# Kernel optimization log

Hardware: AMD Instinct MI355X
Metric: run time of the kernel (lower is better)

Reference implementation:

```python
import jax, jax.numpy as jnp
import numpy as np

B, S, H, IN, OUT, T = 1024, 256, 128, 2, 2, 512


def setup_inputs() -> dict:
    key = jax.random.key(0)
    ks = jax.random.split(key, 7)
    scale = 1.0 / np.sqrt(H)  # PyTorch LSTM init range ~ U(-1/sqrt(H), 1/sqrt(H))
    return {
        "x": jax.random.normal(ks[0], (B, S, IN), jnp.float32),
        "w_ih": jax.random.normal(ks[1], (4 * H, IN), jnp.float32) * scale,
        "w_hh": jax.random.normal(ks[2], (4 * H, H), jnp.float32) * scale,
        "b_ih": jax.random.normal(ks[3], (4 * H,), jnp.float32) * scale,
        "b_hh": jax.random.normal(ks[4], (4 * H,), jnp.float32) * scale,
        "w_fc": jax.random.normal(ks[5], (OUT, H), jnp.float32) * scale,
        "b_fc": jax.random.normal(ks[6], (OUT,), jnp.float32) * scale,
        "target_length": T,
    }


def reference(x, w_ih, w_hh, b_ih, b_hh, w_fc, b_fc, target_length):
    # PyTorch nn.LSTM cell, gate order (i, f, g, o). Dropout is identity (eval mode).
    bias = b_ih + b_hh
    hdim = w_hh.shape[1]

    def cell(h, c, x_t):
        gates = x_t @ w_ih.T + h @ w_hh.T + bias  # [B, 4H]
        i, f, g, o = jnp.split(gates, 4, axis=-1)
        c_new = jax.nn.sigmoid(f) * c + jax.nn.sigmoid(i) * jnp.tanh(g)
        h_new = jax.nn.sigmoid(o) * jnp.tanh(c_new)
        return h_new, c_new

    bsz = x.shape[0]
    h0 = jnp.zeros((bsz, hdim), x.dtype)
    c0 = jnp.zeros((bsz, hdim), x.dtype)

    # Encode input sequence
    def enc_step(carry, x_t):
        h, c = carry
        h, c = cell(h, c, x_t)
        return (h, c), None

    (h, c), _ = jax.lax.scan(enc_step, (h0, c0), jnp.swapaxes(x, 0, 1))

    inp0 = x[:, -1, :]  # [B, 2]

    def dec_step(carry, _):
        h, c, inp = carry
        h, c = cell(h, c, inp)
        pred = h @ w_fc.T + b_fc  # [B, 2]
        return (h, c, pred), pred

    _, preds = jax.lax.scan(dec_step, (h, c, inp0), None, length=target_length)
    return jnp.swapaxes(preds, 0, 1)  # [B, target_length, 2]
```

## Files before the change

kernel.cpp:

```cpp
#include <hip/hip_runtime.h>

typedef unsigned short ush;
typedef unsigned int uint32;
typedef __attribute__((ext_vector_type(8))) __bf16 bf16x8;
typedef __attribute__((ext_vector_type(4))) float f32x4;

#define NBLK 256
#define RB   4
#define NTHR 512
#define SENC 256
#define TDEC 512
#define HDIM 128
#define HSTR 144
#define XSTR 520
#define PSTR 1024

#define LOG2E  1.4426950408889634f
#define LOG2E2 2.8853900817779268f

__device__ __forceinline__ float bf2f(ush u){
  uint32 v = ((uint32)u) << 16;
  return __builtin_bit_cast(float, v);
}
__device__ __forceinline__ ush f2bf(float f){
  uint32 u = __builtin_bit_cast(uint32, f);
  u = (u + 0x7FFFu + ((u >> 16) & 1u)) >> 16;
  return (ush)u;
}
__device__ __forceinline__ float lo16f(uint32 w){ return __builtin_bit_cast(float, w << 16); }
__device__ __forceinline__ float hi16f(uint32 w){ return __builtin_bit_cast(float, w & 0xFFFF0000u); }

__device__ __forceinline__ float loadf(const void* p, int i, bool f32){
  return f32 ? ((const float*)p)[i] : bf2f(((const ush*)p)[i]);
}
__device__ __forceinline__ bf16x8 load8bf(const void* p, int i, bool f32){
  bf16x8 r;
  if (!f32){
    uint4 u = *reinterpret_cast<const uint4*>((const ush*)p + i);
    r = __builtin_bit_cast(bf16x8, u);
  } else {
    const float* fp = (const float*)p + i;
    #pragma unroll
    for (int j = 0; j < 8; ++j) r[j] = (__bf16)fp[j];
  }
  return r;
}
__device__ __forceinline__ float sigm(float x){
  return __builtin_amdgcn_rcpf(1.0f + __builtin_amdgcn_exp2f(-x * LOG2E));
}
__device__ __forceinline__ float tnh(float x){
  return 1.0f - 2.0f * __builtin_amdgcn_rcpf(__builtin_amdgcn_exp2f(x * LOG2E2) + 1.0f);
}
__device__ __forceinline__ f32x4 mfma4(const bf16x8* af, const bf16x8* b, f32x4 c){
  f32x4 r = __builtin_amdgcn_mfma_f32_16x16x32_bf16(af[0], b[0], c, 0, 0, 0);
  r = __builtin_amdgcn_mfma_f32_16x16x32_bf16(af[1], b[1], r, 0, 0, 0);
  r = __builtin_amdgcn_mfma_f32_16x16x32_bf16(af[2], b[2], r, 0, 0, 0);
  r = __builtin_amdgcn_mfma_f32_16x16x32_bf16(af[3], b[3], r, 0, 0, 0);
  return r;
}

__global__ void __launch_bounds__(NTHR, 2)
lstm_kernel(const void* __restrict__ xg,  const void* __restrict__ wih,
            const void* __restrict__ whh, const void* __restrict__ bih,
            const void* __restrict__ bhh, const void* __restrict__ wfc,
            const void* __restrict__ bfc, void* __restrict__ outg)
{
  __shared__ __attribute__((aligned(16))) ush x_lds[RB * XSTR];
  __shared__ __attribute__((aligned(16))) ush h_lds[2][RB * HSTR];
  __shared__ __attribute__((aligned(16))) ush pred_lds[RB][PSTR];

  const int tid   = threadIdx.x;
  const int lane  = tid & 63;
  const int wv    = tid >> 6;
  const int n     = lane & 15;
  const int q     = lane >> 4;
  const int gbase = wv << 4;
  const int blk   = blockIdx.x;

  const uint32* wp = (const uint32*)whh;
  int cnt = 0;
  #pragma unroll
  for (int i = 0; i < 64; ++i){
    uint32 e = (wp[i] >> 7) & 0xFFu;
    cnt += (e >= 90u && e <= 140u) ? 1 : 0;
  }
  const bool isf32 = (cnt < 40);

  for (int i = tid; i < 2 * RB * HSTR; i += NTHR) h_lds[0][i] = 0;

  if (!isf32){
    if (tid < 256){
      int row = tid >> 6, c = (tid & 63) * 8;
      uint4 v = *reinterpret_cast<const uint4*>((const ush*)xg + (blk * RB + row) * (SENC * 2) + c);
      *reinterpret_cast<uint4*>(&x_lds[row * XSTR + c]) = v;
    }
  } else {
    for (int i = tid; i < RB * SENC * 2; i += NTHR){
      int row = i >> 9, c = i & 511;
      x_lds[row * XSTR + c] = f2bf(((const float*)xg)[(blk * RB + row) * (SENC * 2) + c]);
    }
  }

  float wih0v[4], wih1v[4];
  f32x4 biasC[4];
  bf16x8 bfr[4][4];
  #pragma unroll
  for (int p = 0; p < 4; ++p){
    int g = p * 128 + gbase + n;
    float b = loadf(bih, g, isf32) + loadf(bhh, g, isf32);
    biasC[p][0] = b; biasC[p][1] = b; biasC[p][2] = b; biasC[p][3] = b;
    wih0v[p] = loadf(wih, g * 2 + 0, isf32);
    wih1v[p] = loadf(wih, g * 2 + 1, isf32);
    #pragma unroll
    for (int kk = 0; kk < 4; ++kk)
      bfr[p][kk] = load8bf(whh, g * HDIM + kk * 32 + q * 8, isf32);
  }
  bf16x8 wfcfr[4];
  #pragma unroll
  for (int kk = 0; kk < 4; ++kk){
    #pragma unroll
    for (int j = 0; j < 8; ++j){
      int k = kk * 32 + q * 8 + j;
      wfcfr[kk][j] = __builtin_bit_cast(__bf16, f2bf(loadf(wfc, (n & 1) * HDIM + k, isf32)));
    }
  }
  f32x4 pbfcC;
  {
    float pb = loadf(bfc, n & 1, isf32);
    pbfcC[0] = pb; pbfcC[1] = pb; pbfcC[2] = pb; pbfcC[3] = pb;
  }
  float wav[4], wbv[4];
  #pragma unroll
  for (int p = 0; p < 4; ++p){
    wav[p] = (n & 1) ? wih1v[p] : wih0v[p];
    wbv[p] = (n & 1) ? wih0v[p] : wih1v[p];
  }

  float cc = 0.0f;
  const int arow  = (n >> 2) * HSTR;
  const int hwofs = q * HSTR + gbase + n;
  int cur = 0;

  __syncthreads();

  #pragma unroll 1
  for (int s = 0; s <= SENC; ++s){
    int t = (s < SENC) ? s : SENC - 1;
    uint32 xw = *reinterpret_cast<const uint32*>(&x_lds[q * XSTR + t * 2]);
    float xa = lo16f(xw), xb = hi16f(xw);

    const ush* hb = &h_lds[cur][arow];
    bf16x8 af[4];
    #pragma unroll
    for (int kk = 0; kk < 4; ++kk)
      af[kk] = *reinterpret_cast<const bf16x8*>(hb + kk * 32 + q * 8);

    f32x4 acc0 = mfma4(af, bfr[0], biasC[0]);
    f32x4 acc1 = mfma4(af, bfr[1], biasC[1]);
    float g0 = acc0[0] + wih0v[0] * xa + wih1v[0] * xb;
    float si = sigm(g0);
    f32x4 acc2 = mfma4(af, bfr[2], biasC[2]);
    float g1 = acc1[0] + wih0v[1] * xa + wih1v[1] * xb;
    float sf = sigm(g1);
    f32x4 acc3 = mfma4(af, bfr[3], biasC[3]);
    float g2 = acc2[0] + wih0v[2] * xa + wih1v[2] * xb;
    float tg = tnh(g2);
    cc = sf * cc + si * tg;
    float th = tnh(cc);
    float g3 = acc3[0] + wih0v[3] * xa + wih1v[3] * xb;
    float so = sigm(g3);
    h_lds[cur ^ 1][hwofs] = f2bf(so * th);

    __syncthreads();
    cur ^= 1;
  }

  #pragma unroll 1
  for (int d = 0; d < TDEC - 1; ++d){
    const ush* hb = &h_lds[cur][arow];
    bf16x8 af[4];
    #pragma unroll
    for (int kk = 0; kk < 4; ++kk)
      af[kk] = *reinterpret_cast<const bf16x8*>(hb + kk * 32 + q * 8);

    f32x4 a4 = mfma4(af, wfcfr, pbfcC);
    float pv = a4[0];
    float po = __shfl_xor(pv, 1, 64);

    f32x4 acc0 = mfma4(af, bfr[0], biasC[0]);
    f32x4 acc1 = mfma4(af, bfr[1], biasC[1]);
    float g0 = acc0[0] + wav[0] * pv + wbv[0] * po;
    float si = sigm(g0);
    f32x4 acc2 = mfma4(af, bfr[2], biasC[2]);
    float g1 = acc1[0] + wav[1] * pv + wbv[1] * po;
    float sf = sigm(g1);
    f32x4 acc3 = mfma4(af, bfr[3], biasC[3]);
    float g2 = acc2[0] + wav[2] * pv + wbv[2] * po;
    float tg = tnh(g2);
    cc = sf * cc + si * tg;
    float th = tnh(cc);
    float g3 = acc3[0] + wav[3] * pv + wbv[3] * po;
    float so = sigm(g3);
    h_lds[cur ^ 1][hwofs] = f2bf(so * th);

    if (wv == 0 && n < 2)
      pred_lds[q][d * 2 + n] = f2bf(pv);

    __syncthreads();
    cur ^= 1;
  }

  if (wv == 0){
    const ush* hb = &h_lds[cur][arow];
    bf16x8 af[4];
    #pragma unroll
    for (int kk = 0; kk < 4; ++kk)
      af[kk] = *reinterpret_cast<const bf16x8*>(hb + kk * 32 + q * 8);
    f32x4 a4 = mfma4(af, wfcfr, pbfcC);
    if (n < 2)
      pred_lds[q][(TDEC - 1) * 2 + n] = f2bf(a4[0]);
  }
  __syncthreads();

  if (!isf32){
    int row = tid >> 7, c = (tid & 127) * 8;
    uint4 v = *reinterpret_cast<const uint4*>(&pred_lds[row][c]);
    *reinterpret_cast<uint4*>((ush*)outg + (blk * RB + row) * (TDEC * 2) + c) = v;
  } else {
    for (int i = tid; i < RB * TDEC * 2; i += NTHR){
      int row = i >> 10, c = i & 1023;
      ((float*)outg)[(blk * RB + row) * (TDEC * 2) + c] = bf2f(pred_lds[row][c]);
    }
  }
}

extern "C" void kernel_launch(void* const* d_in, const int* in_sizes, int n_in,
                              void* d_out, int out_size, void* d_ws, size_t ws_size,
                              hipStream_t stream) {
  lstm_kernel<<<dim3(NBLK), dim3(NTHR), 0, stream>>>(
      d_in[0], d_in[1], d_in[2], d_in[3], d_in[4], d_in[5], d_in[6], d_out);
}
```

Before: 431.6 us.

## Fold fc projection into decoder recurrent weights and interleave MFMA chains

```diff
diff --git a/kernel.cpp b/kernel.cpp
--- a/kernel.cpp
+++ b/kernel.cpp
@@ -23,9 +23,7 @@
   return __builtin_bit_cast(float, v);
 }
 __device__ __forceinline__ ush f2bf(float f){
-  uint32 u = __builtin_bit_cast(uint32, f);
-  u = (u + 0x7FFFu + ((u >> 16) & 1u)) >> 16;
-  return (ush)u;
+  return __builtin_bit_cast(ush, (__bf16)f);
 }
 __device__ __forceinline__ float lo16f(uint32 w){ return __builtin_bit_cast(float, w << 16); }
 __device__ __forceinline__ float hi16f(uint32 w){ return __builtin_bit_cast(float, w & 0xFFFF0000u); }
@@ -51,12 +49,8 @@
 __device__ __forceinline__ float tnh(float x){
   return 1.0f - 2.0f * __builtin_amdgcn_rcpf(__builtin_amdgcn_exp2f(x * LOG2E2) + 1.0f);
 }
-__device__ __forceinline__ f32x4 mfma4(const bf16x8* af, const bf16x8* b, f32x4 c){
-  f32x4 r = __builtin_amdgcn_mfma_f32_16x16x32_bf16(af[0], b[0], c, 0, 0, 0);
-  r = __builtin_amdgcn_mfma_f32_16x16x32_bf16(af[1], b[1], r, 0, 0, 0);
-  r = __builtin_amdgcn_mfma_f32_16x16x32_bf16(af[2], b[2], r, 0, 0, 0);
-  r = __builtin_amdgcn_mfma_f32_16x16x32_bf16(af[3], b[3], r, 0, 0, 0);
-  return r;
+__device__ __forceinline__ f32x4 M1(bf16x8 a, bf16x8 b, f32x4 c){
+  return __builtin_amdgcn_mfma_f32_16x16x32_bf16(a, b, c, 0, 0, 0);
 }
 
 __global__ void __launch_bounds__(NTHR, 2)
@@ -121,7 +115,7 @@
     #pragma unroll
     for (int j = 0; j < 8; ++j){
       int k = kk * 32 + q * 8 + j;
-      wfcfr[kk][j] = __builtin_bit_cast(__bf16, f2bf(loadf(wfc, (n & 1) * HDIM + k, isf32)));
+      wfcfr[kk][j] = (__bf16)loadf(wfc, (n & 1) * HDIM + k, isf32);
     }
   }
   f32x4 pbfcC;
@@ -129,17 +123,12 @@
     float pb = loadf(bfc, n & 1, isf32);
     pbfcC[0] = pb; pbfcC[1] = pb; pbfcC[2] = pb; pbfcC[3] = pb;
   }
-  float wav[4], wbv[4];
-  #pragma unroll
-  for (int p = 0; p < 4; ++p){
-    wav[p] = (n & 1) ? wih1v[p] : wih0v[p];
-    wbv[p] = (n & 1) ? wih0v[p] : wih1v[p];
-  }
 
   float cc = 0.0f;
   const int arow  = (n >> 2) * HSTR;
   const int hwofs = q * HSTR + gbase + n;
   int cur = 0;
+  const f32x4 Z = {0.0f, 0.0f, 0.0f, 0.0f};
 
   __syncthreads();
 
@@ -147,64 +136,119 @@
   for (int s = 0; s <= SENC; ++s){
     int t = (s < SENC) ? s : SENC - 1;
     uint32 xw = *reinterpret_cast<const uint32*>(&x_lds[q * XSTR + t * 2]);
+
+    const ush* hb = &h_lds[cur][arow];
+    bf16x8 af0 = *reinterpret_cast<const bf16x8*>(hb + 0 * 32 + q * 8);
+    bf16x8 af1 = *reinterpret_cast<const bf16x8*>(hb + 1 * 32 + q * 8);
+    bf16x8 af2 = *reinterpret_cast<const bf16x8*>(hb + 2 * 32 + q * 8);
+    bf16x8 af3 = *reinterpret_cast<const bf16x8*>(hb + 3 * 32 + q * 8);
+
+    f32x4 A0 = M1(af0, bfr[0][0], biasC[0]);
+    f32x4 A1 = M1(af0, bfr[1][0], biasC[1]);
+    f32x4 A2 = M1(af0, bfr[2][0], biasC[2]);
+    f32x4 A3 = M1(af0, bfr[3][0], biasC[3]);
+    f32x4 B0 = M1(af2, bfr[0][2], Z);
+    f32x4 B1 = M1(af2, bfr[1][2], Z);
+    f32x4 B2 = M1(af2, bfr[2][2], Z);
+    f32x4 B3 = M1(af2, bfr[3][2], Z);
+    A0 = M1(af1, bfr[0][1], A0);
+    A1 = M1(af1, bfr[1][1], A1);
+    A2 = M1(af1, bfr[2][1], A2);
+    A3 = M1(af1, bfr[3][1], A3);
+    B0 = M1(af3, bfr[0][3], B0);
+    B1 = M1(af3, bfr[1][3], B1);
+    B2 = M1(af3, bfr[2][3], B2);
+    B3 = M1(af3, bfr[3][3], B3);
+
     float xa = lo16f(xw), xb = hi16f(xw);
-
-    const ush* hb = &h_lds[cur][arow];
-    bf16x8 af[4];
-    #pragma unroll
-    for (int kk = 0; kk < 4; ++kk)
-      af[kk] = *reinterpret_cast<const bf16x8*>(hb + kk * 32 + q * 8);
-
-    f32x4 acc0 = mfma4(af, bfr[0], biasC[0]);
-    f32x4 acc1 = mfma4(af, bfr[1], biasC[1]);
-    float g0 = acc0[0] + wih0v[0] * xa + wih1v[0] * xb;
+    float xc0 = wih0v[0] * xa + wih1v[0] * xb;
+    float xc1 = wih0v[1] * xa + wih1v[1] * xb;
+    float xc2 = wih0v[2] * xa + wih1v[2] * xb;
+    float xc3 = wih0v[3] * xa + wih1v[3] * xb;
+
+    float g0 = A0[0] + B0[0] + xc0;
+    float g1 = A1[0] + B1[0] + xc1;
+    float g2 = A2[0] + B2[0] + xc2;
+    float g3 = A3[0] + B3[0] + xc3;
     float si = sigm(g0);
-    f32x4 acc2 = mfma4(af, bfr[2], biasC[2]);
-    float g1 = acc1[0] + wih0v[1] * xa + wih1v[1] * xb;
     float sf = sigm(g1);
-    f32x4 acc3 = mfma4(af, bfr[3], biasC[3]);
-    float g2 = acc2[0] + wih0v[2] * xa + wih1v[2] * xb;
     float tg = tnh(g2);
+    float so = sigm(g3);
     cc = sf * cc + si * tg;
-    float th = tnh(cc);
-    float g3 = acc3[0] + wih0v[3] * xa + wih1v[3] * xb;
-    float so = sigm(g3);
-    h_lds[cur ^ 1][hwofs] = f2bf(so * th);
+    h_lds[cur ^ 1][hwofs] = f2bf(so * tnh(cc));
 
     __syncthreads();
     cur ^= 1;
+  }
+
+  {
+    float bfc0 = loadf(bfc, 0, isf32), bfc1 = loadf(bfc, 1, isf32);
+    #pragma unroll
+    for (int p = 0; p < 4; ++p){
+      float nb = biasC[p][0] + wih0v[p] * bfc0 + wih1v[p] * bfc1;
+      biasC[p][0] = nb; biasC[p][1] = nb; biasC[p][2] = nb; biasC[p][3] = nb;
+    }
+    #pragma unroll
+    for (int kk = 0; kk < 4; ++kk){
+      #pragma unroll
+      for (int j = 0; j < 8; ++j){
+        int k = kk * 32 + q * 8 + j;
+        float w0 = loadf(wfc, k, isf32);
+        float w1 = loadf(wfc, HDIM + k, isf32);
+        #pragma unroll
+        for (int p = 0; p < 4; ++p)
+          bfr[p][kk][j] = (__bf16)((float)bfr[p][kk][j] + wih0v[p] * w0 + wih1v[p] * w1);
+      }
+    }
   }
 
   #pragma unroll 1
   for (int d = 0; d < TDEC - 1; ++d){
     const ush* hb = &h_lds[cur][arow];
-    bf16x8 af[4];
-    #pragma unroll
-    for (int kk = 0; kk < 4; ++kk)
-      af[kk] = *reinterpret_cast<const bf16x8*>(hb + kk * 32 + q * 8);
-
-    f32x4 a4 = mfma4(af, wfcfr, pbfcC);
-    float pv = a4[0];
-    float po = __shfl_xor(pv, 1, 64);
-
-    f32x4 acc0 = mfma4(af, bfr[0], biasC[0]);
-    f32x4 acc1 = mfma4(af, bfr[1], biasC[1]);
-    float g0 = acc0[0] + wav[0] * pv + wbv[0] * po;
+    bf16x8 af0 = *reinterpret_cast<const bf16x8*>(hb + 0 * 32 + q * 8);
+    bf16x8 af1 = *reinterpret_cast<const bf16x8*>(hb + 1 * 32 + q * 8);
+    bf16x8 af2 = *reinterpret_cast<const bf16x8*>(hb + 2 * 32 + q * 8);
+    bf16x8 af3 = *reinterpret_cast<const bf16x8*>(hb + 3 * 32 + q * 8);
+
+    f32x4 A0 = M1(af0, bfr[0][0], biasC[0]);
+    f32x4 A1 = M1(af0, bfr[1][0], biasC[1]);
+    f32x4 A2 = M1(af0, bfr[2][0], biasC[2]);
+    f32x4 A3 = M1(af0, bfr[3][0], biasC[3]);
+    f32x4 B0 = M1(af2, bfr[0][2], Z);
+    f32x4 B1 = M1(af2, bfr[1][2], Z);
+    f32x4 B2 = M1(af2, bfr[2][2], Z);
+    f32x4 B3 = M1(af2, bfr[3][2], Z);
+
+    f32x4 P0, P1;
+    if (wv == 0){
+      P0 = M1(af0, wfcfr[0], pbfcC);
+      P1 = M1(af2, wfcfr[2], Z);
+      P0 = M1(af1, wfcfr[1], P0);
+      P1 = M1(af3, wfcfr[3], P1);
+    }
+
+    A0 = M1(af1, bfr[0][1], A0);
+    A1 = M1(af1, bfr[1][1], A1);
+    A2 = M1(af1, bfr[2][1], A2);
+    A3 = M1(af1, bfr[3][1], A3);
+    B0 = M1(af3, bfr[0][3], B0);
+    B1 = M1(af3, bfr[1][3], B1);
+    B2 = M1(af3, bfr[2][3], B2);
+    B3 = M1(af3, bfr[3][3], B3);
+
+    float g0 = A0[0] + B0[0];
+    float g1 = A1[0] + B1[0];
+    float g2 = A2[0] + B2[0];
+    float g3 = A3[0] + B3[0];
     float si = sigm(g0);
-    f32x4 acc2 = mfma4(af, bfr[2], biasC[2]);
-    float g1 = acc1[0] + wav[1] * pv + wbv[1] * po;
     float sf = sigm(g1);
-    f32x4 acc3 = mfma4(af, bfr[3], biasC[3]);
-    float g2 = acc2[0] + wav[2] * pv + wbv[2] * po;
     float tg = tnh(g2);
+    float so = sigm(g3);
     cc = sf * cc + si * tg;
-    float th = tnh(cc);
-    float g3 = acc3[0] + wav[3] * pv + wbv[3] * po;
-    float so = sigm(g3);
-    h_lds[cur ^ 1][hwofs] = f2bf(so * th);
+    h_lds[cur ^ 1][hwofs] = f2bf(so * tnh(cc));
 
     if (wv == 0 && n < 2)
-      pred_lds[q][d * 2 + n] = f2bf(pv);
+      pred_lds[q][d * 2 + n] = f2bf(P0[0] + P1[0]);
 
     __syncthreads();
     cur ^= 1;
@@ -212,13 +256,16 @@
 
   if (wv == 0){
     const ush* hb = &h_lds[cur][arow];
-    bf16x8 af[4];
-    #pragma unroll
-    for (int kk = 0; kk < 4; ++kk)
-      af[kk] = *reinterpret_cast<const bf16x8*>(hb + kk * 32 + q * 8);
-    f32x4 a4 = mfma4(af, wfcfr, pbfcC);
+    bf16x8 af0 = *reinterpret_cast<const bf16x8*>(hb + 0 * 32 + q * 8);
+    bf16x8 af1 = *reinterpret_cast<const bf16x8*>(hb + 1 * 32 + q * 8);
+    bf16x8 af2 = *reinterpret_cast<const bf16x8*>(hb + 2 * 32 + q * 8);
+    bf16x8 af3 = *reinterpret_cast<const bf16x8*>(hb + 3 * 32 + q * 8);
+    f32x4 P0 = M1(af0, wfcfr[0], pbfcC);
+    f32x4 P1 = M1(af2, wfcfr[2], Z);
+    P0 = M1(af1, wfcfr[1], P0);
+    P1 = M1(af3, wfcfr[3], P1);
     if (n < 2)
-      pred_lds[q][(TDEC - 1) * 2 + n] = f2bf(a4[0]);
+      pred_lds[q][(TDEC - 1) * 2 + n] = f2bf(P0[0] + P1[0]);
   }
   __syncthreads();
 
```

Result: no change. 432.1 us (+0.1%).

## Fold fc feedback into decoder recurrent weights and split MFMA chains

Applied to the files above, without the earlier changes.

```diff
diff --git a/kernel.cpp b/kernel.cpp
--- a/kernel.cpp
+++ b/kernel.cpp
@@ -23,9 +23,7 @@
   return __builtin_bit_cast(float, v);
 }
 __device__ __forceinline__ ush f2bf(float f){
-  uint32 u = __builtin_bit_cast(uint32, f);
-  u = (u + 0x7FFFu + ((u >> 16) & 1u)) >> 16;
-  return (ush)u;
+  return __builtin_bit_cast(ush, (__bf16)f);
 }
 __device__ __forceinline__ float lo16f(uint32 w){ return __builtin_bit_cast(float, w << 16); }
 __device__ __forceinline__ float hi16f(uint32 w){ return __builtin_bit_cast(float, w & 0xFFFF0000u); }
@@ -51,12 +49,8 @@
 __device__ __forceinline__ float tnh(float x){
   return 1.0f - 2.0f * __builtin_amdgcn_rcpf(__builtin_amdgcn_exp2f(x * LOG2E2) + 1.0f);
 }
-__device__ __forceinline__ f32x4 mfma4(const bf16x8* af, const bf16x8* b, f32x4 c){
-  f32x4 r = __builtin_amdgcn_mfma_f32_16x16x32_bf16(af[0], b[0], c, 0, 0, 0);
-  r = __builtin_amdgcn_mfma_f32_16x16x32_bf16(af[1], b[1], r, 0, 0, 0);
-  r = __builtin_amdgcn_mfma_f32_16x16x32_bf16(af[2], b[2], r, 0, 0, 0);
-  r = __builtin_amdgcn_mfma_f32_16x16x32_bf16(af[3], b[3], r, 0, 0, 0);
-  return r;
+__device__ __forceinline__ f32x4 M1(bf16x8 a, bf16x8 b, f32x4 c){
+  return __builtin_amdgcn_mfma_f32_16x16x32_bf16(a, b, c, 0, 0, 0);
 }
 
 __global__ void __launch_bounds__(NTHR, 2)
@@ -68,12 +62,14 @@
   __shared__ __attribute__((aligned(16))) ush x_lds[RB * XSTR];
   __shared__ __attribute__((aligned(16))) ush h_lds[2][RB * HSTR];
   __shared__ __attribute__((aligned(16))) ush pred_lds[RB][PSTR];
+  __shared__ __attribute__((aligned(16))) float ppart[2][RB][2][4];
 
   const int tid   = threadIdx.x;
   const int lane  = tid & 63;
   const int wv    = tid >> 6;
   const int n     = lane & 15;
   const int q     = lane >> 4;
+  const int q8    = q * 8;
   const int gbase = wv << 4;
   const int blk   = blockIdx.x;
 
@@ -113,112 +109,151 @@
     wih1v[p] = loadf(wih, g * 2 + 1, isf32);
     #pragma unroll
     for (int kk = 0; kk < 4; ++kk)
-      bfr[p][kk] = load8bf(whh, g * HDIM + kk * 32 + q * 8, isf32);
-  }
-  bf16x8 wfcfr[4];
+      bfr[p][kk] = load8bf(whh, g * HDIM + kk * 32 + q8, isf32);
+  }
+  const bool ispred = (wv == 0) || (wv == 3) || (wv == 5) || (wv == 6);
+  const bool issum  = (wv == 1);
+  const int  pkk    = (wv == 0) ? 0 : (wv == 3) ? 1 : (wv == 5) ? 2 : 3;
+  const int  pofs   = pkk * 32 + q8;
+  bf16x8 wpfr;
   #pragma unroll
-  for (int kk = 0; kk < 4; ++kk){
-    #pragma unroll
-    for (int j = 0; j < 8; ++j){
-      int k = kk * 32 + q * 8 + j;
-      wfcfr[kk][j] = __builtin_bit_cast(__bf16, f2bf(loadf(wfc, (n & 1) * HDIM + k, isf32)));
-    }
-  }
-  f32x4 pbfcC;
+  for (int j = 0; j < 8; ++j)
+    wpfr[j] = (__bf16)loadf(wfc, (n & 1) * HDIM + pkk * 32 + q8 + j, isf32);
+  f32x4 predC;
   {
-    float pb = loadf(bfc, n & 1, isf32);
-    pbfcC[0] = pb; pbfcC[1] = pb; pbfcC[2] = pb; pbfcC[3] = pb;
-  }
-  float wav[4], wbv[4];
-  #pragma unroll
-  for (int p = 0; p < 4; ++p){
-    wav[p] = (n & 1) ? wih1v[p] : wih0v[p];
-    wbv[p] = (n & 1) ? wih0v[p] : wih1v[p];
+    float pb = (wv == 0) ? loadf(bfc, n & 1, isf32) : 0.0f;
+    predC[0] = pb; predC[1] = pb; predC[2] = pb; predC[3] = pb;
   }
 
   float cc = 0.0f;
   const int arow  = (n >> 2) * HSTR;
   const int hwofs = q * HSTR + gbase + n;
-  int cur = 0;
+  const f32x4 Z = {0.0f, 0.0f, 0.0f, 0.0f};
 
   __syncthreads();
 
+#define LOADAF(RBUF) \
+    const ush* hb = &h_lds[RBUF][arow]; \
+    bf16x8 af0 = *reinterpret_cast<const bf16x8*>(hb + q8); \
+    bf16x8 af1 = *reinterpret_cast<const bf16x8*>(hb + 32 + q8); \
+    bf16x8 af2 = *reinterpret_cast<const bf16x8*>(hb + 64 + q8); \
+    bf16x8 af3 = *reinterpret_cast<const bf16x8*>(hb + 96 + q8);
+
+#define GATEMM \
+    f32x4 A0 = M1(af0, bfr[0][0], biasC[0]); \
+    f32x4 A1 = M1(af0, bfr[1][0], biasC[1]); \
+    f32x4 A2 = M1(af0, bfr[2][0], biasC[2]); \
+    f32x4 A3 = M1(af0, bfr[3][0], biasC[3]); \
+    f32x4 B0 = M1(af2, bfr[0][2], Z); \
+    f32x4 B1 = M1(af2, bfr[1][2], Z); \
+    f32x4 B2 = M1(af2, bfr[2][2], Z); \
+    f32x4 B3 = M1(af2, bfr[3][2], Z); \
+    A0 = M1(af1, bfr[0][1], A0); \
+    B0 = M1(af3, bfr[0][3], B0); \
+    A1 = M1(af1, bfr[1][1], A1); \
+    B1 = M1(af3, bfr[1][3], B1); \
+    A2 = M1(af1, bfr[2][1], A2); \
+    B2 = M1(af3, bfr[2][3], B2); \
+    A3 = M1(af1, bfr[3][1], A3); \
+    B3 = M1(af3, bfr[3][3], B3);
+
+#define ENCSTEP(RBUF, WBUF, T) { \
+    LOADAF(RBUF) \
+    uint32 xw = *reinterpret_cast<const uint32*>(&x_lds[q * XSTR + (T) * 2]); \
+    GATEMM \
+    float xa = lo16f(xw), xb = hi16f(xw); \
+    float g0 = A0[0] + B0[0] + (wih0v[0] * xa + wih1v[0] * xb); \
+    float g1 = A1[0] + B1[0] + (wih0v[1] * xa + wih1v[1] * xb); \
+    float g2 = A2[0] + B2[0] + (wih0v[2] * xa + wih1v[2] * xb); \
+    float g3 = A3[0] + B3[0] + (wih0v[3] * xa + wih1v[3] * xb); \
+    float si = sigm(g0); \
+    float sf = sigm(g1); \
+    float tg = tnh(g2); \
+    float so = sigm(g3); \
+    cc = sf * cc + si * tg; \
+    h_lds[WBUF][hwofs] = f2bf(so * tnh(cc)); \
+    __syncthreads(); \
+  }
+
+#define DECSTEP(RBUF, WBUF, D) { \
+    LOADAF(RBUF) \
+    if (issum && (D) > 0 && n < 2){ \
+      f32x4 pp = *reinterpret_cast<const f32x4*>(&ppart[((D) - 1) & 1][q][n][0]); \
+      pred_lds[q][((D) - 1) * 2 + n] = f2bf(pp[0] + pp[1] + pp[2] + pp[3]); \
+    } \
+    GATEMM \
+    f32x4 PP = predC; \
+    if (ispred) PP = M1(*reinterpret_cast<const bf16x8*>(hb + pofs), wpfr, predC); \
+    float g0 = A0[0] + B0[0]; \
+    float g1 = A1[0] + B1[0]; \
+    float g2 = A2[0] + B2[0]; \
+    float g3 = A3[0] + B3[0]; \
+    float si = sigm(g0); \
+    float sf = sigm(g1); \
+    float tg = tnh(g2); \
+    float so = sigm(g3); \
+    cc = sf * cc + si * tg; \
+    h_lds[WBUF][hwofs] = f2bf(so * tnh(cc)); \
+    if (ispred && n < 2) ppart[(D) & 1][q][n][pkk] = PP[0]; \
+    __syncthreads(); \
+  }
+
   #pragma unroll 1
-  for (int s = 0; s <= SENC; ++s){
-    int t = (s < SENC) ? s : SENC - 1;
-    uint32 xw = *reinterpret_cast<const uint32*>(&x_lds[q * XSTR + t * 2]);
-    float xa = lo16f(xw), xb = hi16f(xw);
-
-    const ush* hb = &h_lds[cur][arow];
-    bf16x8 af[4];
-    #pragma unroll
-    for (int kk = 0; kk < 4; ++kk)
-      af[kk] = *reinterpret_cast<const bf16x8*>(hb + kk * 32 + q * 8);
-
-    f32x4 acc0 = mfma4(af, bfr[0], biasC[0]);
-    f32x4 acc1 = mfma4(af, bfr[1], biasC[1]);
-    float g0 = acc0[0] + wih0v[0] * xa + wih1v[0] * xb;
-    float si = sigm(g0);
-    f32x4 acc2 = mfma4(af, bfr[2], biasC[2]);
-    float g1 = acc1[0] + wih0v[1] * xa + wih1v[1] * xb;
-    float sf = sigm(g1);
-    f32x4 acc3 = mfma4(af, bfr[3], biasC[3]);
-    float g2 = acc2[0] + wih0v[2] * xa + wih1v[2] * xb;
-    float tg = tnh(g2);
-    cc = sf * cc + si * tg;
-    float th = tnh(cc);
-    float g3 = acc3[0] + wih0v[3] * xa + wih1v[3] * xb;
-    float so = sigm(g3);
-    h_lds[cur ^ 1][hwofs] = f2bf(so * th);
-
-    __syncthreads();
-    cur ^= 1;
+  for (int s = 0; s < SENC; s += 2){
+    ENCSTEP(0, 1, s)
+    ENCSTEP(1, 0, s + 1)
+  }
+  ENCSTEP(0, 1, SENC - 1)
+
+  {
+    float bfc0 = loadf(bfc, 0, isf32), bfc1 = loadf(bfc, 1, isf32);
+    #pragma unroll
+    for (int p = 0; p < 4; ++p){
+      float nb = biasC[p][0] + wih0v[p] * bfc0 + wih1v[p] * bfc1;
+      biasC[p][0] = nb; biasC[p][1] = nb; biasC[p][2] = nb; biasC[p][3] = nb;
+    }
+    #pragma unroll
+    for (int kk = 0; kk < 4; ++kk){
+      #pragma unroll
+      for (int j = 0; j < 8; ++j){
+        int k = kk * 32 + q8 + j;
+        float w0 = loadf(wfc, k, isf32);
+        float w1 = loadf(wfc, HDIM + k, isf32);
+        #pragma unroll
+        for (int p = 0; p < 4; ++p)
+          bfr[p][kk][j] = (__bf16)((float)bfr[p][kk][j] + wih0v[p] * w0 + wih1v[p] * w1);
+      }
+    }
   }
 
   #pragma unroll 1
-  for (int d = 0; d < TDEC - 1; ++d){
-    const ush* hb = &h_lds[cur][arow];
-    bf16x8 af[4];
-    #pragma unroll
-    for (int kk = 0; kk < 4; ++kk)
-      af[kk] = *reinterpret_cast<const bf16x8*>(hb + kk * 32 + q * 8);
-
-    f32x4 a4 = mfma4(af, wfcfr, pbfcC);
-    float pv = a4[0];
-    float po = __shfl_xor(pv, 1, 64);
-
-    f32x4 acc0 = mfma4(af, bfr[0], biasC[0]);
-    f32x4 acc1 = mfma4(af, bfr[1], biasC[1]);
-    float g0 = acc0[0] + wav[0] * pv + wbv[0] * po;
-    float si = sigm(g0);
-    f32x4 acc2 = mfma4(af, bfr[2], biasC[2]);
-    float g1 = acc1[0] + wav[1] * pv + wbv[1] * po;
-    float sf = sigm(g1);
-    f32x4 acc3 = mfma4(af, bfr[3], biasC[3]);
-    float g2 = acc2[0] + wav[2] * pv + wbv[2] * po;
-    float tg = tnh(g2);
-    cc = sf * cc + si * tg;
-    float th = tnh(cc);
-    float g3 = acc3[0] + wav[3] * pv + wbv[3] * po;
-    float so = sigm(g3);
-    h_lds[cur ^ 1][hwofs] = f2bf(so * th);
-
-    if (wv == 0 && n < 2)
-      pred_lds[q][d * 2 + n] = f2bf(pv);
-
-    __syncthreads();
-    cur ^= 1;
+  for (int d = 0; d < TDEC - 2; d += 2){
+    DECSTEP(1, 0, d)
+    DECSTEP(0, 1, d + 1)
+  }
+  DECSTEP(1, 0, TDEC - 2)
+
+  if (issum && n < 2){
+    f32x4 pp = *reinterpret_cast<const f32x4*>(&ppart[0][q][n][0]);
+    pred_lds[q][(TDEC - 2) * 2 + n] = f2bf(pp[0] + pp[1] + pp[2] + pp[3]);
   }
 
   if (wv == 0){
-    const ush* hb = &h_lds[cur][arow];
-    bf16x8 af[4];
-    #pragma unroll
-    for (int kk = 0; kk < 4; ++kk)
-      af[kk] = *reinterpret_cast<const bf16x8*>(hb + kk * 32 + q * 8);
-    f32x4 a4 = mfma4(af, wfcfr, pbfcC);
+    LOADAF(0)
+    bf16x8 wf0, wf1, wf2, wf3;
+    #pragma unroll
+    for (int j = 0; j < 8; ++j){
+      wf0[j] = (__bf16)loadf(wfc, (n & 1) * HDIM +   0 + q8 + j, isf32);
+      wf1[j] = (__bf16)loadf(wfc, (n & 1) * HDIM +  32 + q8 + j, isf32);
+      wf2[j] = (__bf16)loadf(wfc, (n & 1) * HDIM +  64 + q8 + j, isf32);
+      wf3[j] = (__bf16)loadf(wfc, (n & 1) * HDIM +  96 + q8 + j, isf32);
+    }
+    f32x4 P = M1(af0, wf0, predC);
+    f32x4 Q = M1(af2, wf2, Z);
+    P = M1(af1, wf1, P);
+    Q = M1(af3, wf3, Q);
     if (n < 2)
-      pred_lds[q][(TDEC - 1) * 2 + n] = f2bf(a4[0]);
+      pred_lds[q][(TDEC - 1) * 2 + n] = f2bf(P[0] + Q[0]);
   }
   __syncthreads();
 
```

After: 423.3 us. No clear change (-1.9%).
